# Performance work log

Hardware: AMD Instinct MI355X
Metric: run time of the kernel (lower is better)

The kernel has to match this reference:

```python
import jax, jax.numpy as jnp
import numpy as np

T, B = 64, 32
POS_V, WORD_V = 48, 32000
P_EMB, W_EMB = 128, 512
P_HID, W_HID = 256, 1024


def setup_inputs() -> dict:
    key = jax.random.key(0)
    ks = iter(jax.random.split(key, 40))
    def prm(shape, s=0.05):
        return jax.random.normal(next(ks), shape, dtype=jnp.float32) * s
    z = lambda *shape: jnp.zeros(shape, jnp.float32)
    inp = {
        'pos': jax.random.randint(next(ks), (T, B), 0, POS_V),
        'word': jax.random.randint(next(ks), (T, B), 0, WORD_V),
        'pos_emb_W': prm((POS_V, P_EMB)),
        'word_emb_W': prm((WORD_V, W_EMB)),
        'w2p_W': prm((W_HID, W_HID)), 'w2p_b': z(W_HID),
        'p2w_W': prm((P_HID, P_HID)), 'p2w_b': z(P_HID),
        'p_Wih0': prm((4 * P_HID, P_EMB + W_HID)), 'p_Whh0': prm((4 * P_HID, P_HID)),
        'p_bih0': z(4 * P_HID), 'p_bhh0': z(4 * P_HID),
        'w_Wih0': prm((4 * W_HID, W_EMB + P_HID)), 'w_Whh0': prm((4 * W_HID, W_HID)),
        'w_bih0': z(4 * W_HID), 'w_bhh0': z(4 * W_HID),
        'w_Wih1': prm((4 * W_HID, W_HID)), 'w_Whh1': prm((4 * W_HID, W_HID)),
        'w_bih1': z(4 * W_HID), 'w_bhh1': z(4 * W_HID),
        'pos_proj_W': prm((POS_V, P_HID)), 'pos_proj_b': z(POS_V),
        'word_proj1_W': prm((W_EMB, W_HID)), 'word_proj1_b': z(W_EMB),
        'word_proj2_b': z(WORD_V),
    }
    return inp


def _lstm_cell(x, h, c, Wih, Whh, bih, bhh):
    # PyTorch LSTMCell: gates ordered i, f, g, o
    g = x @ Wih.T + h @ Whh.T + bih + bhh
    i, f, gg, o = jnp.split(g, 4, axis=-1)
    c_new = jax.nn.sigmoid(f) * c + jax.nn.sigmoid(i) * jnp.tanh(gg)
    h_new = jax.nn.sigmoid(o) * jnp.tanh(c_new)
    return h_new, c_new


def reference(pos, word, pos_emb_W, word_emb_W, w2p_W, w2p_b, p2w_W, p2w_b,
              p_Wih0, p_Whh0, p_bih0, p_bhh0,
              w_Wih0, w_Whh0, w_bih0, w_bhh0,
              w_Wih1, w_Whh1, w_bih1, w_bhh1,
              pos_proj_W, pos_proj_b, word_proj1_W, word_proj1_b, word_proj2_b):
    p_emb = pos_emb_W[pos]    # [T, B, P_EMB]
    w_emb = word_emb_W[word]  # [T, B, W_EMB]
    Bn = pos.shape[1]
    p_layers = [(p_Wih0, p_Whh0, p_bih0, p_bhh0)]
    w_layers = [(w_Wih0, w_Whh0, w_bih0, w_bhh0), (w_Wih1, w_Whh1, w_bih1, w_bhh1)]
    ph = p_Whh0.shape[1]
    wh = w_Whh0.shape[1]
    init = (jnp.zeros((1, Bn, ph), jnp.float32), jnp.zeros((1, Bn, ph), jnp.float32),
            jnp.zeros((2, Bn, wh), jnp.float32), jnp.zeros((2, Bn, wh), jnp.float32))

    def step(carry, xs):
        p_h, p_c, w_h, w_c = carry
        p_t, w_t = xs
        # word_gate on word-RNN last hidden at t-1, conditions POS-RNN at t
        last_w = jnp.tanh(w_h[-1] @ w2p_W.T + w2p_b)
        x = jnp.concatenate([p_t, last_w], axis=-1)
        new_ph, new_pc = [], []
        for li, (Wih, Whh, bih, bhh) in enumerate(p_layers):
            h, c = _lstm_cell(x, p_h[li], p_c[li], Wih, Whh, bih, bhh)
            new_ph.append(h); new_pc.append(c); x = h
        p_out = jax.nn.log_softmax(x @ pos_proj_W.T + pos_proj_b, axis=-1)
        # pos_gate on POS-RNN last hidden at t, conditions word-RNN at t
        last_p = jnp.tanh(new_ph[-1] @ p2w_W.T + p2w_b)
        x = jnp.concatenate([w_t, last_p], axis=-1)
        new_wh, new_wc = [], []
        for li, (Wih, Whh, bih, bhh) in enumerate(w_layers):
            h, c = _lstm_cell(x, w_h[li], w_c[li], Wih, Whh, bih, bhh)
            new_wh.append(h); new_wc.append(c); x = h
        # tied word projection: hid -> emb -> vocab with embedding weight
        w_logits = (x @ word_proj1_W.T + word_proj1_b) @ word_emb_W.T + word_proj2_b
        w_out = jax.nn.log_softmax(w_logits, axis=-1)
        carry = (jnp.stack(new_ph), jnp.stack(new_pc), jnp.stack(new_wh), jnp.stack(new_wc))
        return carry, (p_out, w_out)

    _, (p_outs, w_outs) = jax.lax.scan(step, init, (p_emb, w_emb))
    return p_outs, w_outs
```

## Files before the change

### kernel.cpp

```cpp
#include <hip/hip_runtime.h>
#include <math.h>

#define LSTR 36

__device__ __forceinline__ void gemm_core(
    const float* __restrict__ A, int lda,
    const float* __restrict__ W, int ldw,
    int n0, int N, int K,
    const float* __restrict__ b1, const float* __restrict__ b2,
    int act, float* __restrict__ C, int ldc, int row0,
    float* As, float* Ws)
{
    const int tid = threadIdx.x;
    const int jl = tid & 15;
    const int bg = tid >> 4;
    float acc[4][4] = {{0.f,0.f,0.f,0.f},{0.f,0.f,0.f,0.f},{0.f,0.f,0.f,0.f},{0.f,0.f,0.f,0.f}};

    for (int kk = 0; kk < K; kk += 32) {
        for (int i = tid; i < 256; i += 128) {
            int r = i >> 3, kv = (i & 7) << 2;
            *(float4*)&As[r * LSTR + kv] =
                *(const float4*)(A + (size_t)(row0 + r) * lda + kk + kv);
        }
        for (int i = tid; i < 512; i += 128) {
            int r = i >> 3, kv = (i & 7) << 2;
            int n = n0 + r;
            float4 val;
            if (n < N) val = *(const float4*)(W + (size_t)n * ldw + kk + kv);
            else       val = make_float4(0.f, 0.f, 0.f, 0.f);
            *(float4*)&Ws[r * LSTR + kv] = val;
        }
        __syncthreads();
#pragma unroll
        for (int k4 = 0; k4 < 8; ++k4) {
            float4 av[4], wv[4];
#pragma unroll
            for (int jb = 0; jb < 4; ++jb) av[jb] = *(float4*)&As[(bg + 8 * jb) * LSTR + k4 * 4];
#pragma unroll
            for (int jn = 0; jn < 4; ++jn) wv[jn] = *(float4*)&Ws[(jl + 16 * jn) * LSTR + k4 * 4];
#pragma unroll
            for (int jn = 0; jn < 4; ++jn)
#pragma unroll
                for (int jb = 0; jb < 4; ++jb) {
                    acc[jn][jb] += av[jb].x * wv[jn].x;
                    acc[jn][jb] += av[jb].y * wv[jn].y;
                    acc[jn][jb] += av[jb].z * wv[jn].z;
                    acc[jn][jb] += av[jb].w * wv[jn].w;
                }
        }
        __syncthreads();
    }

#pragma unroll
    for (int jn = 0; jn < 4; ++jn) {
        int n = n0 + jl + 16 * jn;
        if (n < N) {
            float bb = (b1 ? b1[n] : 0.f) + (b2 ? b2[n] : 0.f);
#pragma unroll
            for (int jb = 0; jb < 4; ++jb) {
                int b = bg + 8 * jb;
                float x = acc[jn][jb] + bb;
                if (act == 1) x = tanhf(x);
                C[(size_t)(row0 + b) * ldc + n] = x;
            }
        }
    }
}

__global__ void __launch_bounds__(128) gemm_generic(
    const float* __restrict__ A, int lda, const float* __restrict__ W, int ldw,
    const float* __restrict__ b1, const float* __restrict__ b2,
    float* __restrict__ C, int ldc, int N, int K, int act, int swapxy)
{
    __shared__ __align__(16) float As[32 * LSTR];
    __shared__ __align__(16) float Ws[64 * LSTR];
    int bn = swapxy ? blockIdx.y : blockIdx.x;
    int bm = swapxy ? blockIdx.x : blockIdx.y;
    gemm_core(A, lda, W, ldw, bn * 64, N, K, b1, b2, act, C, ldc, bm * 32, As, Ws);
}

__global__ void __launch_bounds__(128) step_pre(
    int t, const float* __restrict__ Hw1, const float* __restrict__ Hp,
    const float* __restrict__ h_w0,
    const float* __restrict__ w2p_W, const float* __restrict__ w2p_b,
    const float* __restrict__ p_Whh0,
    const float* __restrict__ w_Whh0, const float* __restrict__ w_Whh1,
    const float* __restrict__ w_bih1, const float* __restrict__ w_bhh1,
    float* __restrict__ u, float* __restrict__ hp_hh,
    float* __restrict__ w0_hh, float* __restrict__ w1_hh)
{
    __shared__ __align__(16) float As[32 * LSTR];
    __shared__ __align__(16) float Ws[64 * LSTR];
    int blk = blockIdx.x;
    const float* hw1 = Hw1 + (size_t)t * 32 * 1024;
    const float* hp  = Hp  + (size_t)t * 32 * 256;
    if (blk < 16)
        gemm_core(hw1, 1024, w2p_W, 1024, blk * 64, 1024, 1024, w2p_b, nullptr, 1, u, 1024, 0, As, Ws);
    else if (blk < 32)
        gemm_core(hp, 256, p_Whh0, 256, (blk - 16) * 64, 1024, 256, nullptr, nullptr, 0, hp_hh, 1024, 0, As, Ws);
    else if (blk < 96)
        gemm_core(h_w0, 1024, w_Whh0, 1024, (blk - 32) * 64, 4096, 1024, nullptr, nullptr, 0, w0_hh, 4096, 0, As, Ws);
    else
        gemm_core(hw1, 1024, w_Whh1, 1024, (blk - 96) * 64, 4096, 1024, w_bih1, w_bhh1, 0, w1_hh, 4096, 0, As, Ws);
}

__global__ void __launch_bounds__(128) lstm_cell(
    const float* __restrict__ A, int K,
    const float* __restrict__ Wih, int ldw, int H,
    const float* __restrict__ addA, int ldA,
    const float* __restrict__ addB, int ldB,
    float* __restrict__ h_out, float* __restrict__ c_state)
{
    __shared__ __align__(16) float As[32 * LSTR];
    __shared__ __align__(16) float Ws[64 * LSTR];
    const int tid = threadIdx.x;
    const int jl = tid & 15;
    const int bg = tid >> 4;
    const int j0 = blockIdx.x * 16;
    float acc[4][4] = {{0.f,0.f,0.f,0.f},{0.f,0.f,0.f,0.f},{0.f,0.f,0.f,0.f},{0.f,0.f,0.f,0.f}};

    for (int kk = 0; kk < K; kk += 32) {
        for (int i = tid; i < 256; i += 128) {
            int r = i >> 3, kv = (i & 7) << 2;
            *(float4*)&As[r * LSTR + kv] = *(const float4*)(A + (size_t)r * K + kk + kv);
        }
        for (int i = tid; i < 512; i += 128) {
            int r = i >> 3, kv = (i & 7) << 2;
            int wrow = (r >> 4) * H + j0 + (r & 15);
            *(float4*)&Ws[r * LSTR + kv] = *(const float4*)(Wih + (size_t)wrow * ldw + kk + kv);
        }
        __syncthreads();
#pragma unroll
        for (int k4 = 0; k4 < 8; ++k4) {
            float4 av[4], wv[4];
#pragma unroll
            for (int jb = 0; jb < 4; ++jb) av[jb] = *(float4*)&As[(bg + 8 * jb) * LSTR + k4 * 4];
#pragma unroll
            for (int jn = 0; jn < 4; ++jn) wv[jn] = *(float4*)&Ws[(jl + 16 * jn) * LSTR + k4 * 4];
#pragma unroll
            for (int jn = 0; jn < 4; ++jn)
#pragma unroll
                for (int jb = 0; jb < 4; ++jb) {
                    acc[jn][jb] += av[jb].x * wv[jn].x;
                    acc[jn][jb] += av[jb].y * wv[jn].y;
                    acc[jn][jb] += av[jb].z * wv[jn].z;
                    acc[jn][jb] += av[jb].w * wv[jn].w;
                }
        }
        __syncthreads();
    }

    const int j = j0 + jl;
#pragma unroll
    for (int jb = 0; jb < 4; ++jb) {
        int b = bg + 8 * jb;
        float g[4];
#pragma unroll
        for (int jn = 0; jn < 4; ++jn) {
            int wrow = jn * H + j;
            float x = acc[jn][jb];
            if (addA) x += addA[(size_t)b * ldA + wrow];
            if (addB) x += addB[(size_t)b * ldB + wrow];
            g[jn] = x;
        }
        float c_old = c_state[b * H + j];
        float ii = 1.f / (1.f + expf(-g[0]));
        float ff = 1.f / (1.f + expf(-g[1]));
        float gg = tanhf(g[2]);
        float oo = 1.f / (1.f + expf(-g[3]));
        float cn = ff * c_old + ii * gg;
        float hn = oo * tanhf(cn);
        c_state[b * H + j] = cn;
        h_out[b * H + j] = hn;
    }
}

__global__ void __launch_bounds__(128) gather_emb(
    const int* __restrict__ pos, const int* __restrict__ word,
    const float* __restrict__ pe, const float* __restrict__ we,
    float* __restrict__ Xp, float* __restrict__ Xw)
{
    int row = blockIdx.x;
    int p = pos[row];
    int w = word[row];
    for (int i = threadIdx.x; i < 128; i += 128)
        Xp[(size_t)row * 128 + i] = pe[(size_t)p * 128 + i];
    for (int i = threadIdx.x; i < 512; i += 128)
        Xw[(size_t)row * 512 + i] = we[(size_t)w * 512 + i];
}

__global__ void __launch_bounds__(256) pos_out_k(
    const float* __restrict__ Hp, const float* __restrict__ W,
    const float* __restrict__ bias, float* __restrict__ out)
{
    int row = blockIdx.x * 4 + (threadIdx.x >> 6);
    int lane = threadIdx.x & 63;
    const float* h = Hp + (size_t)row * 256;
    float logit = -INFINITY;
    if (lane < 48) {
        float s = bias[lane];
        const float* w = W + (size_t)lane * 256;
        for (int k = 0; k < 256; k += 4) {
            s += h[k] * w[k];
            s += h[k + 1] * w[k + 1];
            s += h[k + 2] * w[k + 2];
            s += h[k + 3] * w[k + 3];
        }
        logit = s;
    }
    float m = logit;
    for (int off = 1; off < 64; off <<= 1) m = fmaxf(m, __shfl_xor(m, off));
    float e = (lane < 48) ? expf(logit - m) : 0.f;
    float ssum = e;
    for (int off = 1; off < 64; off <<= 1) ssum += __shfl_xor(ssum, off);
    float ls = m + logf(ssum);
    if (lane < 48) out[(size_t)row * 48 + lane] = logit - ls;
}

__global__ void __launch_bounds__(256) logsoftmax_w(float* __restrict__ out)
{
    __shared__ float red[256];
    int row = blockIdx.x;
    float* p = out + (size_t)row * 32000;
    int tid = threadIdx.x;

    float m = -INFINITY;
    for (int i = tid; i < 32000; i += 256) m = fmaxf(m, p[i]);
    red[tid] = m;
    __syncthreads();
    for (int s = 128; s > 0; s >>= 1) {
        if (tid < s) red[tid] = fmaxf(red[tid], red[tid + s]);
        __syncthreads();
    }
    float M = red[0];
    __syncthreads();

    float s = 0.f;
    for (int i = tid; i < 32000; i += 256) s += expf(p[i] - M);
    red[tid] = s;
    __syncthreads();
    for (int st = 128; st > 0; st >>= 1) {
        if (tid < st) red[tid] += red[tid + st];
        __syncthreads();
    }
    float ls = M + logf(red[0]);

    for (int i = tid; i < 32000; i += 256) p[i] -= ls;
}

extern "C" void kernel_launch(void* const* d_in, const int* in_sizes, int n_in,
                              void* d_out, int out_size, void* d_ws, size_t ws_size,
                              hipStream_t stream)
{
    const int T = 64, B = 32, TB = T * B;

    const int*   pos         = (const int*)d_in[0];
    const int*   word        = (const int*)d_in[1];
    const float* pos_emb_W   = (const float*)d_in[2];
    const float* word_emb_W  = (const float*)d_in[3];
    const float* w2p_W       = (const float*)d_in[4];
    const float* w2p_b       = (const float*)d_in[5];
    const float* p2w_W       = (const float*)d_in[6];
    const float* p2w_b       = (const float*)d_in[7];
    const float* p_Wih0      = (const float*)d_in[8];
    const float* p_Whh0      = (const float*)d_in[9];
    const float* p_bih0      = (const float*)d_in[10];
    const float* p_bhh0      = (const float*)d_in[11];
    const float* w_Wih0      = (const float*)d_in[12];
    const float* w_Whh0      = (const float*)d_in[13];
    const float* w_bih0      = (const float*)d_in[14];
    const float* w_bhh0      = (const float*)d_in[15];
    const float* w_Wih1      = (const float*)d_in[16];
    const float* w_Whh1      = (const float*)d_in[17];
    const float* w_bih1      = (const float*)d_in[18];
    const float* w_bhh1      = (const float*)d_in[19];
    const float* pos_proj_W  = (const float*)d_in[20];
    const float* pos_proj_b  = (const float*)d_in[21];
    const float* word_proj1W = (const float*)d_in[22];
    const float* word_proj1b = (const float*)d_in[23];
    const float* word_proj2b = (const float*)d_in[24];

    float* out   = (float*)d_out;
    float* Pout  = out;
    float* Wout  = out + (size_t)TB * 48;

    float* ws = (float*)d_ws;
    size_t off = 0;
    auto alloc = [&](size_t n) { float* p = ws + off; off += n; return p; };
    float* Xp    = alloc((size_t)TB * 128);
    float* Xw    = alloc((size_t)TB * 512);
    float* Ap    = alloc((size_t)TB * 1024);
    float* Hp    = alloc((size_t)(TB + B) * 256);
    float* Hw1   = alloc((size_t)(TB + B) * 1024);
    float* E     = alloc((size_t)TB * 512);
    float* c_p   = alloc((size_t)B * 256);
    float* h_w0  = alloc((size_t)B * 1024);
    float* c_w0  = alloc((size_t)B * 1024);
    float* c_w1  = alloc((size_t)B * 1024);
    float* u     = alloc((size_t)B * 1024);
    float* v     = alloc((size_t)B * 256);
    float* hp_hh = alloc((size_t)B * 1024);
    float* w0_hh = alloc((size_t)B * 4096);
    float* w1_hh = alloc((size_t)B * 4096);

    float* Aw = Wout;

    hipMemsetAsync(c_p, 0, (size_t)(B * 256 + 3 * B * 1024) * 4, stream);
    hipMemsetAsync(Hp,  0, (size_t)B * 256 * 4, stream);
    hipMemsetAsync(Hw1, 0, (size_t)B * 1024 * 4, stream);

    gather_emb<<<TB, 128, 0, stream>>>(pos, word, pos_emb_W, word_emb_W, Xp, Xw);
    gemm_generic<<<dim3(16, 64), 128, 0, stream>>>(Xp, 128, p_Wih0, 1152,
        p_bih0, p_bhh0, Ap, 1024, 1024, 128, 0, 0);
    gemm_generic<<<dim3(64, 64), 128, 0, stream>>>(Xw, 512, w_Wih0, 768,
        w_bih0, w_bhh0, Aw, 4096, 4096, 512, 0, 0);

    for (int t = 0; t < T; ++t) {
        step_pre<<<160, 128, 0, stream>>>(t, Hw1, Hp, h_w0,
            w2p_W, w2p_b, p_Whh0, w_Whh0, w_Whh1, w_bih1, w_bhh1,
            u, hp_hh, w0_hh, w1_hh);
        lstm_cell<<<16, 128, 0, stream>>>(u, 1024, p_Wih0 + 128, 1152, 256,
            Ap + (size_t)t * 32 * 1024, 1024, hp_hh, 1024,
            Hp + (size_t)(t + 1) * 32 * 256, c_p);
        gemm_generic<<<dim3(4, 1), 128, 0, stream>>>(
            Hp + (size_t)(t + 1) * 32 * 256, 256, p2w_W, 256,
            p2w_b, nullptr, v, 256, 256, 256, 1, 0);
        lstm_cell<<<64, 128, 0, stream>>>(v, 256, w_Wih0 + 512, 768, 1024,
            Aw + (size_t)t * 32 * 4096, 4096, w0_hh, 4096, h_w0, c_w0);
        lstm_cell<<<64, 128, 0, stream>>>(h_w0, 1024, w_Wih1, 1024, 1024,
            nullptr, 0, w1_hh, 4096,
            Hw1 + (size_t)(t + 1) * 32 * 1024, c_w1);
    }

    gemm_generic<<<dim3(8, 64), 128, 0, stream>>>(Hw1 + 32 * 1024, 1024,
        word_proj1W, 1024, word_proj1b, nullptr, E, 512, 512, 1024, 0, 0);
    gemm_generic<<<dim3(64, 500), 128, 0, stream>>>(E, 512, word_emb_W, 512,
        word_proj2b, nullptr, Wout, 32000, 32000, 512, 0, 1);
    logsoftmax_w<<<TB, 256, 0, stream>>>(Wout);
    pos_out_k<<<TB / 4, 256, 0, stream>>>(Hp + 32 * 256, pos_proj_W, pos_proj_b, Pout);
}
```

Baseline: 28.03 ms.

## Register-prefetch next K tile in GEMM/LSTM kernels and use online log-softmax

The GEMM core and the fused LSTM cell kernel now load the next 32-wide K slice of A and W into registers while the current slice is being multiplied from shared memory. This hides global load latency behind the FMA loop at the cost of extra registers. Separately, the word log-softmax is rewritten as a single-pass online max/sum with float4 loads and a merged max-sum reduction, which removes one full pass over each 32000-wide row. The online form adds an extra exp per element whenever the running max changes.

```diff
diff --git a/kernel.cpp b/kernel.cpp
--- a/kernel.cpp
+++ b/kernel.cpp
@@ -16,21 +16,52 @@
     const int bg = tid >> 4;
     float acc[4][4] = {{0.f,0.f,0.f,0.f},{0.f,0.f,0.f,0.f},{0.f,0.f,0.f,0.f},{0.f,0.f,0.f,0.f}};
 
+    float4 ra[2], rw[4];
+
+    int ar[2], akv[2], wr[4], wkv[4];
+#pragma unroll
+    for (int p = 0; p < 2; ++p) {
+        int i = tid + 128 * p;
+        ar[p] = i >> 3; akv[p] = (i & 7) << 2;
+    }
+#pragma unroll
+    for (int p = 0; p < 4; ++p) {
+        int i = tid + 128 * p;
+        wr[p] = i >> 3; wkv[p] = (i & 7) << 2;
+    }
+
+#pragma unroll
+    for (int p = 0; p < 2; ++p)
+        ra[p] = *(const float4*)(A + (size_t)(row0 + ar[p]) * lda + akv[p]);
+#pragma unroll
+    for (int p = 0; p < 4; ++p) {
+        int n = n0 + wr[p];
+        rw[p] = (n < N) ? *(const float4*)(W + (size_t)n * ldw + wkv[p])
+                        : make_float4(0.f, 0.f, 0.f, 0.f);
+    }
+
     for (int kk = 0; kk < K; kk += 32) {
-        for (int i = tid; i < 256; i += 128) {
-            int r = i >> 3, kv = (i & 7) << 2;
-            *(float4*)&As[r * LSTR + kv] =
-                *(const float4*)(A + (size_t)(row0 + r) * lda + kk + kv);
-        }
-        for (int i = tid; i < 512; i += 128) {
-            int r = i >> 3, kv = (i & 7) << 2;
-            int n = n0 + r;
-            float4 val;
-            if (n < N) val = *(const float4*)(W + (size_t)n * ldw + kk + kv);
-            else       val = make_float4(0.f, 0.f, 0.f, 0.f);
-            *(float4*)&Ws[r * LSTR + kv] = val;
-        }
+#pragma unroll
+        for (int p = 0; p < 2; ++p)
+            *(float4*)&As[ar[p] * LSTR + akv[p]] = ra[p];
+#pragma unroll
+        for (int p = 0; p < 4; ++p)
+            *(float4*)&Ws[wr[p] * LSTR + wkv[p]] = rw[p];
         __syncthreads();
+
+        if (kk + 32 < K) {
+            int kn = kk + 32;
+#pragma unroll
+            for (int p = 0; p < 2; ++p)
+                ra[p] = *(const float4*)(A + (size_t)(row0 + ar[p]) * lda + kn + akv[p]);
+#pragma unroll
+            for (int p = 0; p < 4; ++p) {
+                int n = n0 + wr[p];
+                rw[p] = (n < N) ? *(const float4*)(W + (size_t)n * ldw + kn + wkv[p])
+                                : make_float4(0.f, 0.f, 0.f, 0.f);
+            }
+        }
+
 #pragma unroll
         for (int k4 = 0; k4 < 8; ++k4) {
             float4 av[4], wv[4];
@@ -119,17 +150,46 @@
     const int j0 = blockIdx.x * 16;
     float acc[4][4] = {{0.f,0.f,0.f,0.f},{0.f,0.f,0.f,0.f},{0.f,0.f,0.f,0.f},{0.f,0.f,0.f,0.f}};
 
+    float4 ra[2], rw[4];
+    int ar[2], akv[2], wr[4], wkv[4], wrow[4];
+#pragma unroll
+    for (int p = 0; p < 2; ++p) {
+        int i = tid + 128 * p;
+        ar[p] = i >> 3; akv[p] = (i & 7) << 2;
+    }
+#pragma unroll
+    for (int p = 0; p < 4; ++p) {
+        int i = tid + 128 * p;
+        wr[p] = i >> 3; wkv[p] = (i & 7) << 2;
+        wrow[p] = (wr[p] >> 4) * H + j0 + (wr[p] & 15);
+    }
+
+#pragma unroll
+    for (int p = 0; p < 2; ++p)
+        ra[p] = *(const float4*)(A + (size_t)ar[p] * K + akv[p]);
+#pragma unroll
+    for (int p = 0; p < 4; ++p)
+        rw[p] = *(const float4*)(Wih + (size_t)wrow[p] * ldw + wkv[p]);
+
     for (int kk = 0; kk < K; kk += 32) {
-        for (int i = tid; i < 256; i += 128) {
-            int r = i >> 3, kv = (i & 7) << 2;
-            *(float4*)&As[r * LSTR + kv] = *(const float4*)(A + (size_t)r * K + kk + kv);
-        }
-        for (int i = tid; i < 512; i += 128) {
-            int r = i >> 3, kv = (i & 7) << 2;
-            int wrow = (r >> 4) * H + j0 + (r & 15);
-            *(float4*)&Ws[r * LSTR + kv] = *(const float4*)(Wih + (size_t)wrow * ldw + kk + kv);
-        }
+#pragma unroll
+        for (int p = 0; p < 2; ++p)
+            *(float4*)&As[ar[p] * LSTR + akv[p]] = ra[p];
+#pragma unroll
+        for (int p = 0; p < 4; ++p)
+            *(float4*)&Ws[wr[p] * LSTR + wkv[p]] = rw[p];
         __syncthreads();
+
+        if (kk + 32 < K) {
+            int kn = kk + 32;
+#pragma unroll
+            for (int p = 0; p < 2; ++p)
+                ra[p] = *(const float4*)(A + (size_t)ar[p] * K + kn + akv[p]);
+#pragma unroll
+            for (int p = 0; p < 4; ++p)
+                rw[p] = *(const float4*)(Wih + (size_t)wrow[p] * ldw + kn + wkv[p]);
+        }
+
 #pragma unroll
         for (int k4 = 0; k4 < 8; ++k4) {
             float4 av[4], wv[4];
@@ -157,10 +217,10 @@
         float g[4];
 #pragma unroll
         for (int jn = 0; jn < 4; ++jn) {
-            int wrow = jn * H + j;
+            int row = jn * H + j;
             float x = acc[jn][jb];
-            if (addA) x += addA[(size_t)b * ldA + wrow];
-            if (addB) x += addB[(size_t)b * ldB + wrow];
+            if (addA) x += addA[(size_t)b * ldA + row];
+            if (addB) x += addB[(size_t)b * ldB + row];
             g[jn] = x;
         }
         float c_old = c_state[b * H + j];
@@ -219,33 +279,39 @@
 
 __global__ void __launch_bounds__(256) logsoftmax_w(float* __restrict__ out)
 {
-    __shared__ float red[256];
+    __shared__ float redm[256], reds[256];
     int row = blockIdx.x;
     float* p = out + (size_t)row * 32000;
+    float4* p4 = (float4*)p;
     int tid = threadIdx.x;
 
-    float m = -INFINITY;
-    for (int i = tid; i < 32000; i += 256) m = fmaxf(m, p[i]);
-    red[tid] = m;
-    __syncthreads();
-    for (int s = 128; s > 0; s >>= 1) {
-        if (tid < s) red[tid] = fmaxf(red[tid], red[tid + s]);
-        __syncthreads();
-    }
-    float M = red[0];
-    __syncthreads();
-
-    float s = 0.f;
-    for (int i = tid; i < 32000; i += 256) s += expf(p[i] - M);
-    red[tid] = s;
+    float m = -INFINITY, s = 0.f;
+    for (int i = tid; i < 8000; i += 256) {
+        float4 v = p4[i];
+        float x;
+        x = v.x; if (x > m) { s = s * expf(m - x) + 1.f; m = x; } else s += expf(x - m);
+        x = v.y; if (x > m) { s = s * expf(m - x) + 1.f; m = x; } else s += expf(x - m);
+        x = v.z; if (x > m) { s = s * expf(m - x) + 1.f; m = x; } else s += expf(x - m);
+        x = v.w; if (x > m) { s = s * expf(m - x) + 1.f; m = x; } else s += expf(x - m);
+    }
+    redm[tid] = m; reds[tid] = s;
     __syncthreads();
     for (int st = 128; st > 0; st >>= 1) {
-        if (tid < st) red[tid] += red[tid + st];
+        if (tid < st) {
+            float m2 = redm[tid + st], s2 = reds[tid + st];
+            float M = fmaxf(redm[tid], m2);
+            reds[tid] = reds[tid] * expf(redm[tid] - M) + s2 * expf(m2 - M);
+            redm[tid] = M;
+        }
         __syncthreads();
     }
-    float ls = M + logf(red[0]);
-
-    for (int i = tid; i < 32000; i += 256) p[i] -= ls;
+    float ls = redm[0] + logf(reds[0]);
+
+    for (int i = tid; i < 8000; i += 256) {
+        float4 v = p4[i];
+        v.x -= ls; v.y -= ls; v.z -= ls; v.w -= ls;
+        p4[i] = v;
+    }
 }
 
 extern "C" void kernel_launch(void* const* d_in, const int* in_sizes, int n_in,
```

After: 27.00 ms. 1.04x faster.
